# Kernel tuning notes

Hardware: AMD Instinct MI355X
Metric: run time of the kernel (lower is better)

Reference implementation:

```python
import jax, jax.numpy as jnp
import numpy as np

B = 65536
SEM, COL, LAT, K, NL = 768, 64, 64, 256, 3
EPS_LN = 1e-5

def layernorm(x, g, b):
    m = jnp.mean(x, axis=-1, keepdims=True)
    v = jnp.mean((x - m) ** 2, axis=-1, keepdims=True)
    return (x - m) * jax.lax.rsqrt(v + EPS_LN) * g + b

def l2norm(x):
    n = jnp.sqrt(jnp.sum(x * x, axis=-1, keepdims=True))
    return x / jnp.maximum(n, 1e-12)

def setup_inputs() -> dict:
    key = jax.random.key(0)
    ks = jax.random.split(key, 32)
    g = lambda i, shape, s=0.02: jax.random.normal(ks[i], shape, jnp.float32) * s
    inp = {
        'semantic_emb': jax.random.normal(ks[0], (B, SEM), jnp.float32),
        'collab_emb':   jax.random.normal(ks[1], (B, COL), jnp.float32),
        # gate network: Linear(64,128)+LN+ReLU+Linear(128,64)+Sigmoid
        'gate_w1': g(2, (COL, 128)), 'gate_b1': jnp.zeros((128,)),
        'gate_ln_g': jnp.ones((128,)), 'gate_ln_b': jnp.zeros((128,)),
        'gate_w2': g(3, (128, COL)), 'gate_b2': jnp.zeros((COL,)),
        # fusion layernorm over 832
        'fusion_ln_g': jnp.ones((SEM + COL,)), 'fusion_ln_b': jnp.zeros((SEM + COL,)),
        # encoder (no bias): 832->512->256->128->64, SiLU between
        'enc_w1': g(4, (SEM + COL, 512)), 'enc_w2': g(5, (512, 256)),
        'enc_w3': g(6, (256, 128)),       'enc_w4': g(7, (128, LAT)),
        # shared decoder (no bias): 64->128->256->512, SiLU after each
        'dec_w1': g(8, (LAT, 128)), 'dec_w2': g(9, (128, 256)), 'dec_w3': g(10, (256, 512)),
        # semantic head: 512->1536 (+LN,ReLU) ->768
        'sem_w1': g(11, (512, 2 * SEM)), 'sem_b1': jnp.zeros((2 * SEM,)),
        'sem_ln_g': jnp.ones((2 * SEM,)), 'sem_ln_b': jnp.zeros((2 * SEM,)),
        'sem_w2': g(12, (2 * SEM, SEM)), 'sem_b2': jnp.zeros((SEM,)),
        # collab head: 512->256 (+LN,ReLU) ->64
        'col_w1': g(13, (512, 256)), 'col_b1': jnp.zeros((256,)),
        'col_ln_g': jnp.ones((256,)), 'col_ln_b': jnp.zeros((256,)),
        'col_w2': g(14, (256, COL)), 'col_b2': jnp.zeros((COL,)),
        # residual codebooks [n_layers, n_embed, latent_dim]
        'codebooks': jax.random.normal(ks[15], (NL, K, LAT), jnp.float32),
    }
    return inp

def _forward(semantic_emb, collab_emb, gate_w1, gate_b1, gate_ln_g, gate_ln_b,
             gate_w2, gate_b2, fusion_ln_g, fusion_ln_b,
             enc_w1, enc_w2, enc_w3, enc_w4, dec_w1, dec_w2, dec_w3,
             sem_w1, sem_b1, sem_ln_g, sem_ln_b, sem_w2, sem_b2,
             col_w1, col_b1, col_ln_g, col_ln_b, col_w2, col_b2, codebooks):
    # --- gated fusion (dropout inactive at eval) ---
    h = jax.nn.relu(layernorm(collab_emb @ gate_w1 + gate_b1, gate_ln_g, gate_ln_b))
    gate_values = jax.nn.sigmoid(h @ gate_w2 + gate_b2)
    denoised_collab = gate_values * collab_emb
    fused = layernorm(jnp.concatenate([semantic_emb, denoised_collab], axis=-1),
                      fusion_ln_g, fusion_ln_b)
    # --- encoder MLP ---
    z = jax.nn.silu(fused @ enc_w1)
    z = jax.nn.silu(z @ enc_w2)
    z = jax.nn.silu(z @ enc_w3)
    z = z @ enc_w4  # [B, LAT]
    # --- residual quantization (eval: nearest-neighbor, straight-through) ---
    residual = z
    z_q_total = jnp.zeros_like(z)
    cb_loss = jnp.float32(0.0)
    cm_loss = jnp.float32(0.0)
    codes_list = []
    for l in range(NL):
        residual = l2norm(residual)  # normalize_residuals=True
        cb = codebooks[l]  # [K, LAT]
        # argmin ||r - e||^2 == argmax (r.e - 0.5||e||^2)
        score = residual @ cb.T - 0.5 * jnp.sum(cb * cb, axis=-1)
        codes = jnp.argmax(score, axis=-1)  # [B]
        e = cb[codes]  # [B, LAT]
        cb_loss = cb_loss + jnp.mean((e - jax.lax.stop_gradient(residual)) ** 2)
        cm_loss = cm_loss + jnp.mean((jax.lax.stop_gradient(e) - residual) ** 2)
        z_q_layer = residual + jax.lax.stop_gradient(e - residual)  # straight-through
        z_q_total = z_q_total + z_q_layer
        residual = residual - z_q_layer
        codes_list.append(codes)
    codes = jnp.stack(codes_list, axis=1)  # [B, NL]
    # --- dual decoders ---
    s = jax.nn.silu(z_q_total @ dec_w1)
    s = jax.nn.silu(s @ dec_w2)
    s = jax.nn.silu(s @ dec_w3)  # [B, 512]
    sh = jax.nn.relu(layernorm(s @ sem_w1 + sem_b1, sem_ln_g, sem_ln_b))
    semantic_recon = sh @ sem_w2 + sem_b2
    ch = jax.nn.relu(layernorm(s @ col_w1 + col_b1, col_ln_g, col_ln_b))
    collab_recon = ch @ col_w2 + col_b2
    return semantic_recon, collab_recon, z_q_total, codes, cb_loss, cm_loss, gate_values

def reference(semantic_emb, collab_emb, gate_w1, gate_b1, gate_ln_g, gate_ln_b,
              gate_w2, gate_b2, fusion_ln_g, fusion_ln_b,
              enc_w1, enc_w2, enc_w3, enc_w4, dec_w1, dec_w2, dec_w3,
              sem_w1, sem_b1, sem_ln_g, sem_ln_b, sem_w2, sem_b2,
              col_w1, col_b1, col_ln_g, col_ln_b, col_w2, col_b2, codebooks):
    return _forward(semantic_emb, collab_emb, gate_w1, gate_b1, gate_ln_g, gate_ln_b,
                    gate_w2, gate_b2, fusion_ln_g, fusion_ln_b,
                    enc_w1, enc_w2, enc_w3, enc_w4, dec_w1, dec_w2, dec_w3,
                    sem_w1, sem_b1, sem_ln_g, sem_ln_b, sem_w2, sem_b2,
                    col_w1, col_b1, col_ln_g, col_ln_b, col_w2, col_b2, codebooks)
```

## Files before the change

kernel.cpp:

```cpp
#include <hip/hip_runtime.h>
#include <hip/hip_bf16.h>
#include <math.h>

typedef __bf16 bf16;
typedef __attribute__((ext_vector_type(8))) __bf16 v8bf;
typedef __attribute__((ext_vector_type(4))) float v4f;
typedef _Float16 f16;
typedef __attribute__((ext_vector_type(8))) _Float16 v8h;
typedef __attribute__((ext_vector_type(4))) _Float16 v4h;

__device__ __forceinline__ void xcd_swizzle(int& bm, int& bn) {
  const int nx = gridDim.x;
  const int id = blockIdx.y * nx + blockIdx.x;
  const int slot = id >> 3;
  const int row_in = slot / nx;
  const int bmi = (id & 7) * (gridDim.y >> 3) + row_in;
  const int bni = slot - row_in * nx;
  bm = bmi << 7; bn = bni << 7;
}

__global__ void wconv_t(const float* __restrict__ W, bf16* __restrict__ Wt, int Kd, int Nd) {
  int e = blockIdx.x * 256 + threadIdx.x;
  if (e < Kd * Nd) {
    int k = e / Nd, n = e - k * Nd;
    Wt[n * Kd + k] = (bf16)W[e];
  }
}

__global__ void wsplit_t(const float* __restrict__ W, f16* __restrict__ W0,
                         f16* __restrict__ W1, int Kd, int Nd) {
  int e = blockIdx.x * 256 + threadIdx.x;
  if (e < Kd * Nd) {
    int k = e / Nd, n = e - k * Nd;
    float v = W[e] * 2048.0f;
    f16 h0 = (f16)v;
    f16 h1 = (f16)(v - (float)h0);
    W0[n * Kd + k] = h0;
    W1[n * Kd + k] = h1;
  }
}

__global__ void cbt_k(const float* __restrict__ cb, float* __restrict__ cbT) {
  int e = blockIdx.x * 256 + threadIdx.x;
  if (e < 3 * 256 * 64) {
    int l = e >> 14, rem = e & 16383;
    int c = rem >> 6, d = rem & 63;
    cbT[l * 16384 + d * 256 + c] = cb[e];
  }
}

__global__ void nhn_k(const float* __restrict__ cb, float* __restrict__ nhn) {
  int l = blockIdx.x, c = threadIdx.x;
  const float* p = cb + l * 16384 + c * 64;
  double s = 0.0;
  for (int d = 0; d < 64; ++d) { double v = (double)p[d]; s += v * v; }
  nhn[l * 256 + c] = (float)(-0.5 * s);
}

template <int EPI>
__global__ __launch_bounds__(256, 2) void sgemm128(
    const float* __restrict__ A, const float* __restrict__ W,
    const float* __restrict__ bias, const float* __restrict__ lng,
    const float* __restrict__ lnb, float* __restrict__ C, int N, int Kd) {
  __shared__ float As[32][132];
  __shared__ float Bs[32][128];
  const int tid = threadIdx.x;
  const int w = tid >> 6, l = tid & 63;
  int tx, ty;
  if (EPI == 2) { tx = tid & 15; ty = tid >> 4; }
  else { tx = ((w & 1) << 3) | (l & 7); ty = ((w >> 1) << 3) | (l >> 3); }
  int bm, bn;
  xcd_swizzle(bm, bn);

  float acc[8][8];
#pragma unroll
  for (int i = 0; i < 8; ++i)
#pragma unroll
    for (int j = 0; j < 8; ++j) acc[i][j] = 0.0f;

  for (int k0 = 0; k0 < Kd; k0 += 32) {
    __syncthreads();
#pragma unroll
    for (int jj = 0; jj < 4; ++jj) {
      int p = tid + 256 * jj;
      int arow = p >> 3, aks = (p & 7) << 2;
      float4 v = *(const float4*)(A + (size_t)(bm + arow) * Kd + k0 + aks);
      As[aks][arow] = v.x; As[aks + 1][arow] = v.y;
      As[aks + 2][arow] = v.z; As[aks + 3][arow] = v.w;
      int bk = p >> 5, bns = (p & 31) << 2;
      float4 u = *(const float4*)(W + (size_t)(k0 + bk) * N + bn + bns);
      *(float4*)(&Bs[bk][bns]) = u;
    }
    __syncthreads();
    float cacc[8][8];
#pragma unroll
    for (int i = 0; i < 8; ++i)
#pragma unroll
      for (int j = 0; j < 8; ++j) cacc[i][j] = 0.0f;
#pragma unroll 4
    for (int kk = 0; kk < 32; ++kk) {
      float a[8], b[8];
#pragma unroll
      for (int i = 0; i < 8; ++i) a[i] = As[kk][ty * 8 + i];
#pragma unroll
      for (int j = 0; j < 8; ++j) b[j] = Bs[kk][tx * 8 + j];
#pragma unroll
      for (int i = 0; i < 8; ++i)
#pragma unroll
        for (int j = 0; j < 8; ++j) cacc[i][j] = fmaf(a[i], b[j], cacc[i][j]);
    }
#pragma unroll
    for (int i = 0; i < 8; ++i)
#pragma unroll
      for (int j = 0; j < 8; ++j) acc[i][j] += cacc[i][j];
  }

  const int colb = bn + tx * 8;
  if (EPI == 0) {
#pragma unroll
    for (int i = 0; i < 8; ++i) {
      int row = bm + ty * 8 + i;
      float o[8];
#pragma unroll
      for (int j = 0; j < 8; ++j) { float v = acc[i][j]; o[j] = v / (1.0f + expf(-v)); }
      *(float4*)(C + (size_t)row * N + colb) = make_float4(o[0], o[1], o[2], o[3]);
      *(float4*)(C + (size_t)row * N + colb + 4) = make_float4(o[4], o[5], o[6], o[7]);
    }
  } else if (EPI == 1) {
    float bb[8];
#pragma unroll
    for (int j = 0; j < 8; ++j) bb[j] = bias[colb + j];
#pragma unroll
    for (int i = 0; i < 8; ++i) {
      int row = bm + ty * 8 + i;
      float o[8];
#pragma unroll
      for (int j = 0; j < 8; ++j) o[j] = acc[i][j] + bb[j];
      *(float4*)(C + (size_t)row * N + colb) = make_float4(o[0], o[1], o[2], o[3]);
      *(float4*)(C + (size_t)row * N + colb + 4) = make_float4(o[4], o[5], o[6], o[7]);
    }
  } else {
    float bb[8], lg[8], lb[8];
#pragma unroll
    for (int j = 0; j < 8; ++j) { bb[j] = bias[colb + j]; lg[j] = lng[colb + j]; lb[j] = lnb[colb + j]; }
#pragma unroll
    for (int i = 0; i < 8; ++i) {
      int row = bm + ty * 8 + i;
      float v[8]; float s = 0.0f;
#pragma unroll
      for (int j = 0; j < 8; ++j) { v[j] = acc[i][j] + bb[j]; s += v[j]; }
      s += __shfl_xor(s, 1); s += __shfl_xor(s, 2); s += __shfl_xor(s, 4); s += __shfl_xor(s, 8);
      float mean = s * (1.0f / 128.0f);
      float ss = 0.0f;
#pragma unroll
      for (int j = 0; j < 8; ++j) { float t = v[j] - mean; ss += t * t; }
      ss += __shfl_xor(ss, 1); ss += __shfl_xor(ss, 2); ss += __shfl_xor(ss, 4); ss += __shfl_xor(ss, 8);
      float rs = 1.0f / sqrtf(ss * (1.0f / 128.0f) + 1e-5f);
      float o[8];
#pragma unroll
      for (int j = 0; j < 8; ++j) o[j] = fmaxf((v[j] - mean) * rs * lg[j] + lb[j], 0.0f);
      *(float4*)(C + (size_t)row * N + colb) = make_float4(o[0], o[1], o[2], o[3]);
      *(float4*)(C + (size_t)row * N + colb + 4) = make_float4(o[4], o[5], o[6], o[7]);
    }
  }
}

template <int EPI>
__global__ __launch_bounds__(256, 2) void sgemm64(
    const float* __restrict__ A, const float* __restrict__ W,
    const float* __restrict__ bias, const float* __restrict__ aux,
    float* __restrict__ C, float* __restrict__ C2, int Kd) {
  __shared__ float As[32][132];
  __shared__ float Bs[32][64];
  const int tid = threadIdx.x;
  const int tx = tid & 15, ty = tid >> 4;
  const int bm = blockIdx.x << 7;

  float acc[8][4];
#pragma unroll
  for (int i = 0; i < 8; ++i)
#pragma unroll
    for (int j = 0; j < 4; ++j) acc[i][j] = 0.0f;

  for (int k0 = 0; k0 < Kd; k0 += 32) {
    __syncthreads();
#pragma unroll
    for (int jj = 0; jj < 4; ++jj) {
      int p = tid + 256 * jj;
      int arow = p >> 3, aks = (p & 7) << 2;
      float4 v = *(const float4*)(A + (size_t)(bm + arow) * Kd + k0 + aks);
      As[aks][arow] = v.x; As[aks + 1][arow] = v.y;
      As[aks + 2][arow] = v.z; As[aks + 3][arow] = v.w;
    }
#pragma unroll
    for (int jj = 0; jj < 2; ++jj) {
      int p = tid + 256 * jj;
      int bk = p >> 4, bns = (p & 15) << 2;
      float4 u = *(const float4*)(W + (size_t)(k0 + bk) * 64 + bns);
      *(float4*)(&Bs[bk][bns]) = u;
    }
    __syncthreads();
    float cacc[8][4];
#pragma unroll
    for (int i = 0; i < 8; ++i)
#pragma unroll
      for (int j = 0; j < 4; ++j) cacc[i][j] = 0.0f;
#pragma unroll 4
    for (int kk = 0; kk < 32; ++kk) {
      float a[8], b[4];
#pragma unroll
      for (int i = 0; i < 8; ++i) a[i] = As[kk][ty * 8 + i];
#pragma unroll
      for (int j = 0; j < 4; ++j) b[j] = Bs[kk][tx * 4 + j];
#pragma unroll
      for (int i = 0; i < 8; ++i)
#pragma unroll
        for (int j = 0; j < 4; ++j) cacc[i][j] = fmaf(a[i], b[j], cacc[i][j]);
    }
#pragma unroll
    for (int i = 0; i < 8; ++i)
#pragma unroll
      for (int j = 0; j < 4; ++j) acc[i][j] += cacc[i][j];
  }

  const int colb = tx * 4;
  if (EPI == 0) {
#pragma unroll
    for (int i = 0; i < 8; ++i) {
      int row = bm + ty * 8 + i;
      float ss = 0.0f;
#pragma unroll
      for (int j = 0; j < 4; ++j) ss += acc[i][j] * acc[i][j];
      ss += __shfl_xor(ss, 1); ss += __shfl_xor(ss, 2); ss += __shfl_xor(ss, 4); ss += __shfl_xor(ss, 8);
      float nrm = fmaxf(sqrtf(ss), 1e-12f);
      *(float4*)(C + (size_t)row * 64 + colb) =
          make_float4(acc[i][0] / nrm, acc[i][1] / nrm, acc[i][2] / nrm, acc[i][3] / nrm);
    }
  } else if (EPI == 1) {
    float bb[4];
#pragma unroll
    for (int j = 0; j < 4; ++j) bb[j] = bias[colb + j];
#pragma unroll
    for (int i = 0; i < 8; ++i) {
      int row = bm + ty * 8 + i;
      *(float4*)(C + (size_t)row * 64 + colb) =
          make_float4(acc[i][0] + bb[0], acc[i][1] + bb[1], acc[i][2] + bb[2], acc[i][3] + bb[3]);
    }
  } else {
    float bb[4];
#pragma unroll
    for (int j = 0; j < 4; ++j) bb[j] = bias[colb + j];
#pragma unroll
    for (int i = 0; i < 8; ++i) {
      int row = bm + ty * 8 + i;
      float4 av = *(const float4*)(aux + (size_t)row * 64 + colb);
      float g[4];
#pragma unroll
      for (int j = 0; j < 4; ++j) g[j] = 1.0f / (1.0f + expf(-(acc[i][j] + bb[j])));
      *(float4*)(C + (size_t)row * 64 + colb) = make_float4(g[0], g[1], g[2], g[3]);
      *(float4*)(C2 + (size_t)row * 64 + colb) =
          make_float4(g[0] * av.x, g[1] * av.y, g[2] * av.z, g[3] * av.w);
    }
  }
}

__global__ __launch_bounds__(256) void fuse_ln(
    const float* __restrict__ sem, const float* __restrict__ den,
    const float* __restrict__ fg, const float* __restrict__ fb,
    float* __restrict__ fused) {
  const int w = threadIdx.x >> 6, l = threadIdx.x & 63;
  float fgv[13], fbv[13];
#pragma unroll
  for (int q = 0; q < 12; ++q) { fgv[q] = fg[q * 64 + l]; fbv[q] = fb[q * 64 + l]; }
  fgv[12] = fg[768 + l]; fbv[12] = fb[768 + l];
  for (int it = 0; it < 4; ++it) {
    int r = (blockIdx.x * 4 + w) * 4 + it;
    float sv[12];
#pragma unroll
    for (int q = 0; q < 12; ++q) sv[q] = sem[(size_t)r * 768 + q * 64 + l];
    float dv = den[(size_t)r * 64 + l];
    float s = dv;
#pragma unroll
    for (int q = 0; q < 12; ++q) s += sv[q];
#pragma unroll
    for (int m = 1; m < 64; m <<= 1) s += __shfl_xor(s, m, 64);
    float mean = s * (1.0f / 832.0f);
    float t0 = dv - mean;
    float ss = t0 * t0;
#pragma unroll
    for (int q = 0; q < 12; ++q) { float t = sv[q] - mean; ss += t * t; }
#pragma unroll
    for (int m = 1; m < 64; m <<= 1) ss += __shfl_xor(ss, m, 64);
    float sc = 1.0f / sqrtf(ss * (1.0f / 832.0f) + 1e-5f);
#pragma unroll
    for (int q = 0; q < 12; ++q)
      fused[(size_t)r * 832 + q * 64 + l] = (sv[q] - mean) * sc * fgv[q] + fbv[q];
    fused[(size_t)r * 832 + 768 + l] = t0 * sc * fgv[12] + fbv[12];
  }
}

template <int LAYER>
__global__ __launch_bounds__(256) void argupd(
    const float* __restrict__ scores, const float* __restrict__ cbl,
    float* __restrict__ rn, float* __restrict__ zq, float* __restrict__ codes,
    float* __restrict__ loss, bf16* __restrict__ zqb) {
  const int w = threadIdx.x >> 6, l = threadIdx.x & 63;
  const int base = (blockIdx.x * 4 + w) * 16;
  float lacc = 0.0f;
  for (int it = 0; it < 16; ++it) {
    int r = base + it;
    float4 s4 = *(const float4*)(scores + (size_t)r * 256 + l * 4);
    float bs = s4.x; int bi = l * 4;
    if (s4.y > bs) { bs = s4.y; bi = l * 4 + 1; }
    if (s4.z > bs) { bs = s4.z; bi = l * 4 + 2; }
    if (s4.w > bs) { bs = s4.w; bi = l * 4 + 3; }
#pragma unroll
    for (int m = 1; m < 64; m <<= 1) {
      float os = __shfl_xor(bs, m, 64);
      int oi = __shfl_xor(bi, m, 64);
      if (os > bs || (os == bs && oi < bi)) { bs = os; bi = oi; }
    }
    float e = cbl[bi * 64 + l];
    float rl = rn[(size_t)r * 64 + l];
    float emr = e - rl;
    float zql = rl + emr;
    lacc += emr * emr;
    if (l == 0) codes[r * 3 + LAYER] = (float)bi;
    if (LAYER == 0) {
      zq[(size_t)r * 64 + l] = zql;
    } else if (LAYER == 1) {
      zq[(size_t)r * 64 + l] += zql;
    } else {
      float tot = zq[(size_t)r * 64 + l] + zql;
      zq[(size_t)r * 64 + l] = tot;
      zqb[(size_t)r * 64 + l] = (bf16)tot;
    }
    if (LAYER < 2) {
      float rnew = rl - zql;
      float ss = rnew * rnew;
#pragma unroll
      for (int m = 1; m < 64; m <<= 1) ss += __shfl_xor(ss, m, 64);
      float nrm = fmaxf(sqrtf(ss), 1e-12f);
      rn[(size_t)r * 64 + l] = rnew / nrm;
    }
  }
#pragma unroll
  for (int m = 1; m < 64; m <<= 1) lacc += __shfl_xor(lacc, m, 64);
  if (l == 0) {
    float v = lacc * (1.0f / 4194304.0f);
    atomicAdd(loss, v);
    atomicAdd(loss + 1, v);
  }
}

typedef __attribute__((address_space(3))) void lds_void_t;
typedef __attribute__((address_space(1))) const void gbl_void_t;
__device__ __forceinline__ void gl_lds16(const void* g, void* l) {
  __builtin_amdgcn_global_load_lds((gbl_void_t*)g, (lds_void_t*)l, 16, 0, 0);
}

__global__ __launch_bounds__(256, 3) void hgemm3(
    const float* __restrict__ A, const f16* __restrict__ W0,
    const f16* __restrict__ W1, float* __restrict__ C, int N, int Kd) {
  __shared__ __align__(16) f16 As0[128 * 32];
  __shared__ __align__(16) f16 As1[128 * 32];
  __shared__ __align__(16) f16 Bs0[128 * 32];
  __shared__ __align__(16) f16 Bs1[128 * 32];
  const int tid = threadIdx.x;
  const int w = tid >> 6, l = tid & 63;
  int bm, bn;
  xcd_swizzle(bm, bn);
  const int wm = (w >> 1) << 6, wn = (w & 1) << 6;

  v4f acc[4][4];
  v4f z4 = {0.0f, 0.0f, 0.0f, 0.0f};
#pragma unroll
  for (int i = 0; i < 4; ++i)
#pragma unroll
    for (int j = 0; j < 4; ++j) acc[i][j] = z4;

  const int srow = (w << 5) + (l >> 2);
  const int skc = (l & 3) << 3;
  const f16* gb0 = W0 + (size_t)(bn + srow) * Kd + skc;
  const f16* gb1 = W1 + (size_t)(bn + srow) * Kd + skc;
  char* lb0 = (char*)Bs0 + (w << 11);
  char* lb1 = (char*)Bs1 + (w << 11);

  for (int k0 = 0; k0 < Kd; k0 += 32) {
    __syncthreads();
    gl_lds16(gb0 + k0, lb0);
    gl_lds16(gb0 + (size_t)16 * Kd + k0, lb0 + 1024);
    gl_lds16(gb1 + k0, lb1);
    gl_lds16(gb1 + (size_t)16 * Kd + k0, lb1 + 1024);
#pragma unroll
    for (int jj = 0; jj < 4; ++jj) {
      int idx = tid + 256 * jj;
      int row = idx >> 3, kq = (idx & 7) << 2;
      float4 v = *(const float4*)(A + (size_t)(bm + row) * Kd + k0 + kq);
      v4h h0, h1;
      float x;
      x = v.x * 256.0f; h0.x = (f16)x; h1.x = (f16)(x - (float)h0.x);
      x = v.y * 256.0f; h0.y = (f16)x; h1.y = (f16)(x - (float)h0.y);
      x = v.z * 256.0f; h0.z = (f16)x; h1.z = (f16)(x - (float)h0.z);
      x = v.w * 256.0f; h0.w = (f16)x; h1.w = (f16)(x - (float)h0.w);
      *(v4h*)(&As0[row * 32 + kq]) = h0;
      *(v4h*)(&As1[row * 32 + kq]) = h1;
    }
    __syncthreads();
    v8h a0f[4], a1f[4], b0f[4], b1f[4];
#pragma unroll
    for (int f = 0; f < 4; ++f) {
      int ro = (wm + f * 16 + (l & 15)) * 32 + ((l >> 4) << 3);
      int co = (wn + f * 16 + (l & 15)) * 32 + ((l >> 4) << 3);
      a0f[f] = *(const v8h*)(As0 + ro);
      a1f[f] = *(const v8h*)(As1 + ro);
      b0f[f] = *(const v8h*)(Bs0 + co);
      b1f[f] = *(const v8h*)(Bs1 + co);
    }
#pragma unroll
    for (int mf = 0; mf < 4; ++mf)
#pragma unroll
      for (int nf = 0; nf < 4; ++nf) {
        acc[mf][nf] = __builtin_amdgcn_mfma_f32_16x16x32_f16(a0f[mf], b1f[nf], acc[mf][nf], 0, 0, 0);
        acc[mf][nf] = __builtin_amdgcn_mfma_f32_16x16x32_f16(a1f[mf], b0f[nf], acc[mf][nf], 0, 0, 0);
        acc[mf][nf] = __builtin_amdgcn_mfma_f32_16x16x32_f16(a0f[mf], b0f[nf], acc[mf][nf], 0, 0, 0);
      }
  }

  const float sc = 1.0f / (256.0f * 2048.0f);
  const int cbase = bn + wn + (l & 15);
#pragma unroll
  for (int mf = 0; mf < 4; ++mf) {
#pragma unroll
    for (int i = 0; i < 4; ++i) {
      int row = bm + wm + mf * 16 + ((l >> 4) << 2) + i;
#pragma unroll
      for (int nf = 0; nf < 4; ++nf) {
        int col = cbase + nf * 16;
        float v = acc[mf][nf][i] * sc;
        v = v / (1.0f + expf(-v));
        C[(size_t)row * N + col] = v;
      }
    }
  }
}

template <int EPI>
__global__ __launch_bounds__(256, 3) void bgemm(
    const bf16* __restrict__ A, const bf16* __restrict__ Wt,
    const float* __restrict__ bias, void* __restrict__ Cv, int N, int Kd) {
  __shared__ __align__(16) bf16 As[128 * 32];
  __shared__ __align__(16) bf16 Bs[128 * 32];
  const int tid = threadIdx.x;
  const int w = tid >> 6, l = tid & 63;
  int bm, bn;
  xcd_swizzle(bm, bn);
  const int wm = (w >> 1) << 6, wn = (w & 1) << 6;

  v4f acc[4][4];
  v4f z4 = {0.0f, 0.0f, 0.0f, 0.0f};
#pragma unroll
  for (int i = 0; i < 4; ++i)
#pragma unroll
    for (int j = 0; j < 4; ++j) acc[i][j] = z4;

  const int srow = (w << 5) + (l >> 2);
  const int skc = (l & 3) << 3;
  const bf16* ga0 = A + (size_t)(bm + srow) * Kd + skc;
  const bf16* gb0 = Wt + (size_t)(bn + srow) * Kd + skc;
  char* la0 = (char*)As + (w << 11);
  char* lb0 = (char*)Bs + (w << 11);

  for (int k0 = 0; k0 < Kd; k0 += 32) {
    __syncthreads();
    gl_lds16(ga0 + k0, la0);
    gl_lds16(ga0 + (size_t)16 * Kd + k0, la0 + 1024);
    gl_lds16(gb0 + k0, lb0);
    gl_lds16(gb0 + (size_t)16 * Kd + k0, lb0 + 1024);
    __syncthreads();
    v8bf af[4], bfr[4];
#pragma unroll
    for (int f = 0; f < 4; ++f) {
      af[f] = *(const v8bf*)(As + (wm + f * 16 + (l & 15)) * 32 + ((l >> 4) << 3));
      bfr[f] = *(const v8bf*)(Bs + (wn + f * 16 + (l & 15)) * 32 + ((l >> 4) << 3));
    }
#pragma unroll
    for (int mf = 0; mf < 4; ++mf)
#pragma unroll
      for (int nf = 0; nf < 4; ++nf)
        acc[mf][nf] = __builtin_amdgcn_mfma_f32_16x16x32_bf16(af[mf], bfr[nf], acc[mf][nf], 0, 0, 0);
  }

  const int cbase = bn + wn + (l & 15);
  float bb[4];
  if (EPI != 0) {
#pragma unroll
    for (int nf = 0; nf < 4; ++nf) bb[nf] = bias[cbase + nf * 16];
  }
#pragma unroll
  for (int mf = 0; mf < 4; ++mf) {
#pragma unroll
    for (int i = 0; i < 4; ++i) {
      int row = bm + wm + mf * 16 + ((l >> 4) << 2) + i;
#pragma unroll
      for (int nf = 0; nf < 4; ++nf) {
        int col = cbase + nf * 16;
        float v = acc[mf][nf][i];
        if (EPI == 0) {
          v = v / (1.0f + __expf(-v));
          ((bf16*)Cv)[(size_t)row * N + col] = (bf16)v;
        } else if (EPI == 1) {
          v += bb[nf];
          ((bf16*)Cv)[(size_t)row * N + col] = (bf16)v;
        } else {
          v += bb[nf];
          ((float*)Cv)[(size_t)row * N + col] = v;
        }
      }
    }
  }
}

template <int VPT, typename T>
__global__ __launch_bounds__(256) void ln_relu(T* __restrict__ x,
    const float* __restrict__ g, const float* __restrict__ b) {
  const int N = VPT * 256;
  const size_t base = (size_t)blockIdx.x * N;
  const int tid = threadIdx.x, w = tid >> 6, l = tid & 63;
  float v[VPT];
#pragma unroll
  for (int q = 0; q < VPT; ++q) v[q] = (float)x[base + q * 256 + tid];
  float s = 0.0f;
#pragma unroll
  for (int q = 0; q < VPT; ++q) s += v[q];
#pragma unroll
  for (int m = 1; m < 64; m <<= 1) s += __shfl_xor(s, m, 64);
  __shared__ float red[8];
  if (l == 0) red[w] = s;
  __syncthreads();
  float mean = (red[0] + red[1] + red[2] + red[3]) * (1.0f / N);
  float ss = 0.0f;
#pragma unroll
  for (int q = 0; q < VPT; ++q) { float t = v[q] - mean; ss += t * t; }
#pragma unroll
  for (int m = 1; m < 64; m <<= 1) ss += __shfl_xor(ss, m, 64);
  if (l == 0) red[4 + w] = ss;
  __syncthreads();
  float var = (red[4] + red[5] + red[6] + red[7]) * (1.0f / N);
  float rs = 1.0f / sqrtf(var + 1e-5f);
#pragma unroll
  for (int q = 0; q < VPT; ++q) {
    int j = q * 256 + tid;
    float y = (v[q] - mean) * rs * g[j] + b[j];
    x[base + j] = (T)fmaxf(y, 0.0f);
  }
}

extern "C" void kernel_launch(void* const* d_in, const int* in_sizes, int n_in,
                              void* d_out, int out_size, void* d_ws, size_t ws_size,
                              hipStream_t stream) {
  (void)in_sizes; (void)n_in; (void)out_size; (void)ws_size;
  const float* semI  = (const float*)d_in[0];
  const float* colI  = (const float*)d_in[1];
  const float* gw1   = (const float*)d_in[2];
  const float* gb1   = (const float*)d_in[3];
  const float* glng  = (const float*)d_in[4];
  const float* glnb  = (const float*)d_in[5];
  const float* gw2   = (const float*)d_in[6];
  const float* gb2   = (const float*)d_in[7];
  const float* fg    = (const float*)d_in[8];
  const float* fb    = (const float*)d_in[9];
  const float* ew1   = (const float*)d_in[10];
  const float* ew2   = (const float*)d_in[11];
  const float* ew3   = (const float*)d_in[12];
  const float* ew4   = (const float*)d_in[13];
  const float* dw1   = (const float*)d_in[14];
  const float* dw2   = (const float*)d_in[15];
  const float* dw3   = (const float*)d_in[16];
  const float* sw1   = (const float*)d_in[17];
  const float* sb1   = (const float*)d_in[18];
  const float* slng  = (const float*)d_in[19];
  const float* slnb  = (const float*)d_in[20];
  const float* sw2   = (const float*)d_in[21];
  const float* sb2   = (const float*)d_in[22];
  const float* cw1   = (const float*)d_in[23];
  const float* cb1   = (const float*)d_in[24];
  const float* clng  = (const float*)d_in[25];
  const float* clnb  = (const float*)d_in[26];
  const float* cw2   = (const float*)d_in[27];
  const float* cb2   = (const float*)d_in[28];
  const float* cbk   = (const float*)d_in[29];

  float* out = (float*)d_out;
  char* ws = (char*)d_ws;

  const size_t OUT_SEM = 0, OUT_COL = 50331648, OUT_ZQ = 54525952,
               OUT_CODES = 58720256, OUT_CB = 58916864, OUT_GATE = 58916866;

  bf16* dec1t = (bf16*)(ws + 0);
  bf16* dec2t = (bf16*)(ws + 16384);
  bf16* dec3t = (bf16*)(ws + 81920);
  bf16* sem1t = (bf16*)(ws + 344064);
  bf16* sem2t = (bf16*)(ws + 1916928);
  bf16* col1t = (bf16*)(ws + 4276224);
  float* cbT  = (float*)(ws + 4538368);
  float* nhn  = (float*)(ws + 4734976);
  f16* e1w0   = (f16*)(ws + 4739072);
  f16* e1w1   = (f16*)(ws + 5591040);
  f16* e2w0   = (f16*)(ws + 6443008);
  f16* e2w1   = (f16*)(ws + 6705152);
  f16* e3w0   = (f16*)(ws + 6967296);
  f16* e3w1   = (f16*)(ws + 7032832);
  const size_t WS_A = 8388608, WS_B = 226492416;
  float* fused  = (float*)(ws + WS_A);
  float* scores = (float*)(ws + WS_A);
  bf16*  semh   = (bf16*)(ws + WS_A);
  float* den = (float*)(ws + WS_B);
  float* hn  = (float*)(ws + WS_B + 16777216);
  float* h1  = (float*)(ws + WS_B);
  float* h2  = (float*)(ws + 360710144);
  float* h3  = (float*)(ws + 427819008);
  float* rn  = (float*)(ws + 461373440);
  bf16* zqb  = (bf16*)(ws + WS_B);
  bf16* d1b  = (bf16*)(ws + WS_B + 8388608);
  bf16* d2b  = (bf16*)(ws + WS_B + 25165824);
  bf16* sb   = (bf16*)(ws + WS_B + 58720256);
  float* colh = (float*)(ws + WS_B + 125829120);

  hipMemsetAsync(out + OUT_CB, 0, 2 * sizeof(float), stream);

  wconv_t<<<(64 * 128 + 255) / 256, 256, 0, stream>>>(dw1, dec1t, 64, 128);
  wconv_t<<<(128 * 256 + 255) / 256, 256, 0, stream>>>(dw2, dec2t, 128, 256);
  wconv_t<<<(256 * 512 + 255) / 256, 256, 0, stream>>>(dw3, dec3t, 256, 512);
  wconv_t<<<(512 * 1536 + 255) / 256, 256, 0, stream>>>(sw1, sem1t, 512, 1536);
  wconv_t<<<(1536 * 768 + 255) / 256, 256, 0, stream>>>(sw2, sem2t, 1536, 768);
  wconv_t<<<(512 * 256 + 255) / 256, 256, 0, stream>>>(cw1, col1t, 512, 256);
  wsplit_t<<<(832 * 512 + 255) / 256, 256, 0, stream>>>(ew1, e1w0, e1w1, 832, 512);
  wsplit_t<<<(512 * 256 + 255) / 256, 256, 0, stream>>>(ew2, e2w0, e2w1, 512, 256);
  wsplit_t<<<(256 * 128 + 255) / 256, 256, 0, stream>>>(ew3, e3w0, e3w1, 256, 128);
  cbt_k<<<192, 256, 0, stream>>>(cbk, cbT);
  nhn_k<<<3, 256, 0, stream>>>(cbk, nhn);

  sgemm128<2><<<dim3(1, 512), 256, 0, stream>>>(colI, gw1, gb1, glng, glnb, hn, 128, 64);
  sgemm64<2><<<512, 256, 0, stream>>>(hn, gw2, gb2, colI, out + OUT_GATE, den, 128);
  fuse_ln<<<4096, 256, 0, stream>>>(semI, den, fg, fb, fused);

  hgemm3<<<dim3(4, 512), 256, 0, stream>>>(fused, e1w0, e1w1, h1, 512, 832);
  hgemm3<<<dim3(2, 512), 256, 0, stream>>>(h1, e2w0, e2w1, h2, 256, 512);
  hgemm3<<<dim3(1, 512), 256, 0, stream>>>(h2, e3w0, e3w1, h3, 128, 256);
  sgemm64<0><<<512, 256, 0, stream>>>(h3, ew4, nullptr, nullptr, rn, nullptr, 128);

  sgemm128<1><<<dim3(2, 512), 256, 0, stream>>>(rn, cbT + 0 * 16384, nhn + 0, nullptr, nullptr, scores, 256, 64);
  argupd<0><<<1024, 256, 0, stream>>>(scores, cbk + 0 * 16384, rn, out + OUT_ZQ, out + OUT_CODES, out + OUT_CB, zqb);
  sgemm128<1><<<dim3(2, 512), 256, 0, stream>>>(rn, cbT + 1 * 16384, nhn + 256, nullptr, nullptr, scores, 256, 64);
  argupd<1><<<1024, 256, 0, stream>>>(scores, cbk + 1 * 16384, rn, out + OUT_ZQ, out + OUT_CODES, out + OUT_CB, zqb);
  sgemm128<1><<<dim3(2, 512), 256, 0, stream>>>(rn, cbT + 2 * 16384, nhn + 512, nullptr, nullptr, scores, 256, 64);
  argupd<2><<<1024, 256, 0, stream>>>(scores, cbk + 2 * 16384, rn, out + OUT_ZQ, out + OUT_CODES, out + OUT_CB, zqb);

  bgemm<0><<<dim3(1, 512), 256, 0, stream>>>(zqb, dec1t, nullptr, d1b, 128, 64);
  bgemm<0><<<dim3(2, 512), 256, 0, stream>>>(d1b, dec2t, nullptr, d2b, 256, 128);
  bgemm<0><<<dim3(4, 512), 256, 0, stream>>>(d2b, dec3t, nullptr, sb, 512, 256);
  bgemm<1><<<dim3(12, 512), 256, 0, stream>>>(sb, sem1t, sb1, semh, 1536, 512);
  ln_relu<6, bf16><<<65536, 256, 0, stream>>>(semh, slng, slnb);
  bgemm<2><<<dim3(6, 512), 256, 0, stream>>>(semh, sem2t, sb2, out + OUT_SEM, 768, 1536);
  bgemm<2><<<dim3(2, 512), 256, 0, stream>>>(sb, col1t, cb1, colh, 256, 512);
  ln_relu<1, float><<<65536, 256, 0, stream>>>(colh, clng, clnb);
  sgemm64<1><<<512, 256, 0, stream>>>(colh, cw2, cb2, nullptr, out + OUT_COL, nullptr, 256);
}
```

Baseline: 2.020 ms.

## Add 256x256 eight-wave pipelined bf16 GEMM for decoder and head layers

Adds a new bf16 MFMA GEMM with 256x256 block tiles and 512 threads. It uses 128KB of swizzled, double-buffered LDS, and its phased barrier schedule interleaves global-to-LDS staging with quarter-tile MFMA bursts under raised wave priority. The kernel replaces the 128x128 bgemm for five decoder and head GEMMs. The larger tiles are meant to raise operand reuse and hide load latency behind compute. In exchange there are fewer blocks, high LDS use that limits occupancy, and a fragile hand-tuned vmcnt and barrier choreography.

```diff
diff --git a/kernel.cpp b/kernel.cpp
--- a/kernel.cpp
+++ b/kernel.cpp
@@ -17,6 +17,16 @@
   const int bmi = (id & 7) * (gridDim.y >> 3) + row_in;
   const int bni = slot - row_in * nx;
   bm = bmi << 7; bn = bni << 7;
+}
+
+__device__ __forceinline__ void xcd_swizzle256(int& bm, int& bn) {
+  const int nx = gridDim.x;
+  const int id = blockIdx.y * nx + blockIdx.x;
+  const int slot = id >> 3;
+  const int row_in = slot / nx;
+  const int bmi = (id & 7) * (gridDim.y >> 3) + row_in;
+  const int bni = slot - row_in * nx;
+  bm = bmi << 8; bn = bni << 8;
 }
 
 __global__ void wconv_t(const float* __restrict__ W, bf16* __restrict__ Wt, int Kd, int Nd) {
@@ -519,6 +529,164 @@
       }
     }
   }
+}
+
+__device__ __forceinline__ void stage_half(const bf16* __restrict__ src, int Kd,
+                                           int rbase, int k0, char* hb8,
+                                           int wid, int l) {
+#pragma unroll
+  for (int j = 0; j < 2; ++j) {
+    int Cc = wid * 128 + j * 64 + l;
+    int cc = Cc ^ (((Cc >> 3) & 3) << 1);
+    gl_lds16(src + (size_t)(rbase + (cc >> 3)) * Kd + k0 + (cc & 7) * 8,
+             hb8 + wid * 2048 + j * 1024);
+  }
+}
+
+__device__ __forceinline__ v8bf ldsfrag(const char* base, int row, int kb) {
+  int p = row * 128 + kb;
+  p ^= ((p >> 7) & 3) << 5;
+  return *(const v8bf*)(base + p);
+}
+
+__device__ __forceinline__ void rd_a(v8bf (&af)[2][4], const char* ab, int mh, int l) {
+  const int rb = mh * 64 + (l & 15);
+  const int kb = (l >> 4) * 16;
+#pragma unroll
+  for (int ks = 0; ks < 2; ++ks)
+#pragma unroll
+    for (int mf = 0; mf < 4; ++mf)
+      af[ks][mf] = ldsfrag(ab, rb + mf * 16, ks * 64 + kb);
+}
+
+__device__ __forceinline__ void rd_b(v8bf (&bfr)[2][2], const char* bbp, int nh, int wl, int l) {
+  const int rb = wl + nh * 32 + (l & 15);
+  const int kb = (l >> 4) * 16;
+#pragma unroll
+  for (int ks = 0; ks < 2; ++ks)
+#pragma unroll
+    for (int nf = 0; nf < 2; ++nf)
+      bfr[ks][nf] = ldsfrag(bbp, rb + nf * 16, ks * 64 + kb);
+}
+
+__device__ __forceinline__ void qmfma(v4f (&q)[4][2], const v8bf (&af)[2][4],
+                                      const v8bf (&bfr)[2][2]) {
+  __builtin_amdgcn_s_setprio(1);
+#pragma unroll
+  for (int ks = 0; ks < 2; ++ks)
+#pragma unroll
+    for (int mf = 0; mf < 4; ++mf)
+#pragma unroll
+      for (int nf = 0; nf < 2; ++nf)
+        q[mf][nf] = __builtin_amdgcn_mfma_f32_16x16x32_bf16(af[ks][mf], bfr[ks][nf],
+                                                            q[mf][nf], 0, 0, 0);
+  __builtin_amdgcn_s_setprio(0);
+}
+
+#define PHASE_BAR() do { __builtin_amdgcn_s_barrier(); __builtin_amdgcn_sched_barrier(0); } while (0)
+
+template <int EPI>
+__global__ __launch_bounds__(512, 2) void bgemm8(
+    const bf16* __restrict__ A, const bf16* __restrict__ Wt,
+    const float* __restrict__ bias, void* __restrict__ Cv, int N, int Kd) {
+  __shared__ __align__(16) char smem[131072];
+  const int tid = threadIdx.x;
+  const int wid = tid >> 6, l = tid & 63;
+  int bm, bn;
+  xcd_swizzle256(bm, bn);
+  const int ha = wid >> 2;
+  const int hbv = (wid & 3) >> 1;
+  const int wl = (wid & 1) * 64;
+  const int NT = Kd >> 6;
+
+  v4f acc[2][2][4][2];
+  v4f z4 = {0.0f, 0.0f, 0.0f, 0.0f};
+#pragma unroll
+  for (int a = 0; a < 2; ++a)
+#pragma unroll
+    for (int b = 0; b < 2; ++b)
+#pragma unroll
+      for (int c = 0; c < 4; ++c)
+#pragma unroll
+        for (int d = 0; d < 2; ++d) acc[a][b][c][d] = z4;
+
+  stage_half(A,  Kd, bm,       0,  smem + 0,     wid, l);
+  stage_half(A,  Kd, bm + 128, 0,  smem + 16384, wid, l);
+  stage_half(Wt, Kd, bn,       0,  smem + 32768, wid, l);
+  stage_half(Wt, Kd, bn + 128, 0,  smem + 49152, wid, l);
+  stage_half(A,  Kd, bm,       64, smem + 65536, wid, l);
+  stage_half(A,  Kd, bm + 128, 64, smem + 81920, wid, l);
+  asm volatile("s_waitcnt vmcnt(4)" ::: "memory");
+  PHASE_BAR();
+
+  for (int K = 0; K < NT; ++K) {
+    const int cur = K & 1;
+    const char* ab = smem + cur * 65536 + ha * 16384;
+    const char* bb = smem + cur * 65536 + 32768 + hbv * 16384;
+    char* stB = smem + ((K + 1) & 1) * 65536 + 32768;
+    char* stA = smem + cur * 65536;
+    const int kB = (K + 1 < NT) ? (K + 1) << 6 : 0;
+    const int kA = (K + 2 < NT) ? (K + 2) << 6 : 0;
+    v8bf a0[2][4], a1[2][4], b0[2][2], b1[2][2];
+
+    rd_a(a0, ab, 0, l);
+    rd_b(b0, bb, 0, wl, l);
+    stage_half(Wt, Kd, bn, kB, stB, wid, l);
+    PHASE_BAR();
+    qmfma(acc[0][0], a0, b0);
+    PHASE_BAR();
+    rd_b(b1, bb, 1, wl, l);
+    stage_half(Wt, Kd, bn + 128, kB, stB + 16384, wid, l);
+    PHASE_BAR();
+    qmfma(acc[0][1], a0, b1);
+    PHASE_BAR();
+    rd_a(a1, ab, 1, l);
+    PHASE_BAR();
+    qmfma(acc[1][0], a1, b0);
+    PHASE_BAR();
+    stage_half(A, Kd, bm, kA, stA, wid, l);
+    stage_half(A, Kd, bm + 128, kA, stA + 16384, wid, l);
+    PHASE_BAR();
+    qmfma(acc[1][1], a1, b1);
+    asm volatile("s_waitcnt vmcnt(4)" ::: "memory");
+    PHASE_BAR();
+  }
+  asm volatile("s_waitcnt vmcnt(0)" ::: "memory");
+
+  const int r0 = bm + ha * 128 + ((l >> 4) << 2);
+  const int c0 = bn + (wid & 3) * 64 + (l & 15);
+  float bb4[2][2];
+  if (EPI != 0) {
+#pragma unroll
+    for (int nh = 0; nh < 2; ++nh)
+#pragma unroll
+      for (int nf = 0; nf < 2; ++nf) bb4[nh][nf] = bias[c0 + nh * 32 + nf * 16];
+  }
+#pragma unroll
+  for (int mh = 0; mh < 2; ++mh)
+#pragma unroll
+    for (int mf = 0; mf < 4; ++mf)
+#pragma unroll
+      for (int i = 0; i < 4; ++i) {
+        const int row = r0 + mh * 64 + mf * 16 + i;
+#pragma unroll
+        for (int nh = 0; nh < 2; ++nh)
+#pragma unroll
+          for (int nf = 0; nf < 2; ++nf) {
+            const int col = c0 + nh * 32 + nf * 16;
+            float v = acc[mh][nh][mf][nf][i];
+            if (EPI == 0) {
+              v = v / (1.0f + __expf(-v));
+              ((bf16*)Cv)[(size_t)row * N + col] = (bf16)v;
+            } else if (EPI == 1) {
+              v += bb4[nh][nf];
+              ((bf16*)Cv)[(size_t)row * N + col] = (bf16)v;
+            } else {
+              v += bb4[nh][nf];
+              ((float*)Cv)[(size_t)row * N + col] = v;
+            }
+          }
+      }
 }
 
 template <int VPT, typename T>
@@ -658,12 +826,12 @@
   argupd<2><<<1024, 256, 0, stream>>>(scores, cbk + 2 * 16384, rn, out + OUT_ZQ, out + OUT_CODES, out + OUT_CB, zqb);
 
   bgemm<0><<<dim3(1, 512), 256, 0, stream>>>(zqb, dec1t, nullptr, d1b, 128, 64);
-  bgemm<0><<<dim3(2, 512), 256, 0, stream>>>(d1b, dec2t, nullptr, d2b, 256, 128);
-  bgemm<0><<<dim3(4, 512), 256, 0, stream>>>(d2b, dec3t, nullptr, sb, 512, 256);
-  bgemm<1><<<dim3(12, 512), 256, 0, stream>>>(sb, sem1t, sb1, semh, 1536, 512);
+  bgemm8<0><<<dim3(1, 256), 512, 0, stream>>>(d1b, dec2t, nullptr, d2b, 256, 128);
+  bgemm8<0><<<dim3(2, 256), 512, 0, stream>>>(d2b, dec3t, nullptr, sb, 512, 256);
+  bgemm8<1><<<dim3(6, 256), 512, 0, stream>>>(sb, sem1t, sb1, semh, 1536, 512);
   ln_relu<6, bf16><<<65536, 256, 0, stream>>>(semh, slng, slnb);
-  bgemm<2><<<dim3(6, 512), 256, 0, stream>>>(semh, sem2t, sb2, out + OUT_SEM, 768, 1536);
-  bgemm<2><<<dim3(2, 512), 256, 0, stream>>>(sb, col1t, cb1, colh, 256, 512);
+  bgemm8<2><<<dim3(3, 256), 512, 0, stream>>>(semh, sem2t, sb2, out + OUT_SEM, 768, 1536);
+  bgemm8<2><<<dim3(1, 256), 512, 0, stream>>>(sb, col1t, cb1, colh, 256, 512);
   ln_relu<1, float><<<65536, 256, 0, stream>>>(colh, clng, clnb);
   sgemm64<1><<<512, 256, 0, stream>>>(colh, cw2, cb2, nullptr, out + OUT_COL, nullptr, 256);
 }
```

Result: faster. 1.941 ms (-3.9%).
